# Kernel tuning notes

Measured on AMD Instinct MI355X. Metric: run time of the kernel, lower is better.

The kernel has to match this reference:

```python
import jax, jax.numpy as jnp
import numpy as np

N = 8192
IN_DIM = 256
OUT_DIM = 128
ALPHA = 0.2  # LeakyReLU negative slope
MASK_VAL = -9e15


def setup_inputs() -> dict:
    key = jax.random.key(0)
    k1, k2, k3, k4 = jax.random.split(key, 4)
    adjacency = jax.random.randint(k1, (N, N), 0, 2, dtype=jnp.int32)
    X = jax.random.normal(k2, (N, IN_DIM), dtype=jnp.float32)
    # kaiming-normal-ish scale
    W = jax.random.normal(k3, (IN_DIM, OUT_DIM), dtype=jnp.float32) * np.sqrt(2.0 / IN_DIM)
    a = jax.random.normal(k4, (2 * OUT_DIM, 1), dtype=jnp.float32) * np.sqrt(2.0 / (2 * OUT_DIM))
    return {"adjacency": adjacency, "X": X, "W": W, "a": a}


def reference(adjacency, X, W, a):
    Wh = X @ W  # [N, D]
    # e[i,j] = lrelu([Wh_i ; Wh_j] @ a) = lrelu(Wh@a1 + (Wh@a2)^T)
    a1 = a[:OUT_DIM, 0]   # [D]
    a2 = a[OUT_DIM:, 0]   # [D]
    e = (Wh @ a1)[:, None] + (Wh @ a2)[None, :]  # [N, N]
    e = jax.nn.leaky_relu(e, negative_slope=ALPHA)
    scores = jnp.where(adjacency > 0, e, jnp.asarray(MASK_VAL, e.dtype))
    attention = jax.nn.softmax(scores, axis=1)  # dropout p=0 -> identity
    h_prime = attention @ Wh  # [N, D]
    return jax.nn.elu(h_prime)
```

## Files before the change

### kernel.cpp

```cpp
#include <hip/hip_runtime.h>
#include <hip/hip_bf16.h>

#define NN 8192
#define KDIM 256
#define DDIM 128

typedef __attribute__((ext_vector_type(8))) short short8;
typedef __attribute__((ext_vector_type(4))) float floatx4;
typedef __attribute__((ext_vector_type(4))) int intx4;

__device__ __forceinline__ unsigned short f2bf(float x) {
    unsigned int u = __float_as_uint(x);
    return (unsigned short)((u + 0x8000u) >> 16);
}

__global__ void k_trip(float* out, float v) {
    if (threadIdx.x == 0 && blockIdx.x == 0) out[0] = v;
}

__global__ void kA_swizzleW(const float* __restrict__ W, unsigned short* __restrict__ WB) {
    int gid = blockIdx.x * blockDim.x + threadIdx.x;
    int kt = gid >> 9, nt = (gid >> 6) & 7, lane = gid & 63;
    int quad = lane >> 4, c = lane & 15;
    short8 pack;
#pragma unroll
    for (int t = 0; t < 8; ++t)
        pack[t] = (short)f2bf(W[(kt * 32 + quad * 8 + t) * DDIM + nt * 16 + c]);
    *(short8*)(WB + ((size_t)(kt * 8 + nt) * 64 + lane) * 8) = pack;
}

__global__ __launch_bounds__(256) void kB_wh(
        const float* __restrict__ X,
        const unsigned short* __restrict__ WB,
        const float* __restrict__ a,
        unsigned short* __restrict__ WhB,
        float* __restrict__ f, float* __restrict__ g) {
    __shared__ unsigned short tile[64 * 128];
    int tid = threadIdx.x;
    int wave = tid >> 6, lane = tid & 63;
    int quad = lane >> 4, c = lane & 15;
    int rowbase = blockIdx.x * 64 + wave * 16;

    floatx4 acc[8];
#pragma unroll
    for (int nt = 0; nt < 8; ++nt) acc[nt] = (floatx4)(0.0f);

    const short8* WB8 = (const short8*)WB;
#pragma unroll
    for (int ks = 0; ks < 8; ++ks) {
        const float* xp = X + (size_t)(rowbase + c) * KDIM + ks * 32 + quad * 8;
        floatx4 x0 = *(const floatx4*)xp;
        floatx4 x1 = *(const floatx4*)(xp + 4);
        short8 afrag;
#pragma unroll
        for (int t = 0; t < 4; ++t) { afrag[t] = (short)f2bf(x0[t]); afrag[4 + t] = (short)f2bf(x1[t]); }
#pragma unroll
        for (int nt = 0; nt < 8; ++nt) {
            short8 b = WB8[(ks * 8 + nt) * 64 + lane];
            acc[nt] = __builtin_amdgcn_mfma_f32_16x16x32_bf16(afrag, b, acc[nt], 0, 0, 0);
        }
    }

    float fp[4] = {0.f, 0.f, 0.f, 0.f}, gp[4] = {0.f, 0.f, 0.f, 0.f};
#pragma unroll
    for (int nt = 0; nt < 8; ++nt) {
        float a1 = a[nt * 16 + c];
        float a2 = a[DDIM + nt * 16 + c];
#pragma unroll
        for (int r = 0; r < 4; ++r) {
            fp[r] += acc[nt][r] * a1;
            gp[r] += acc[nt][r] * a2;
        }
    }
#pragma unroll
    for (int m = 1; m < 16; m <<= 1) {
#pragma unroll
        for (int r = 0; r < 4; ++r) {
            fp[r] += __shfl_xor(fp[r], m);
            gp[r] += __shfl_xor(gp[r], m);
        }
    }
    if (c == 0) {
#pragma unroll
        for (int r = 0; r < 4; ++r) {
            f[rowbase + quad * 4 + r] = fp[r];
            g[rowbase + quad * 4 + r] = gp[r];
        }
    }

#pragma unroll
    for (int nt = 0; nt < 8; ++nt)
#pragma unroll
        for (int r = 0; r < 4; ++r)
            tile[(wave * 16 + quad * 4 + r) * 128 + nt * 16 + c] = f2bf(acc[nt][r]);
    __syncthreads();

    int kt2 = wave >> 1;
#pragma unroll
    for (int ntj = 0; ntj < 4; ++ntj) {
        int nt = (wave & 1) * 4 + ntj;
        short8 pack;
#pragma unroll
        for (int t = 0; t < 8; ++t)
            pack[t] = (short)tile[(kt2 * 32 + quad * 8 + t) * 128 + nt * 16 + c];
        *(short8*)(WhB + ((size_t)((blockIdx.x * 2 + kt2) * 8 + nt) * 64 + lane) * 8) = pack;
    }
}

__global__ __launch_bounds__(256, 3) void kC_attn(
        const int* __restrict__ adj,
        const unsigned short* __restrict__ WhB,
        const float* __restrict__ f, const float* __restrict__ g,
        float* __restrict__ out) {
    __shared__ float smem[8192];
    int tid = threadIdx.x;
    int wave = tid >> 6, lane = tid & 63;
    int quad = lane >> 4, c = lane & 15;
    int rowbase = blockIdx.x * 16;

    for (int i = tid; i < NN / 4; i += 256)
        ((floatx4*)smem)[i] = ((const floatx4*)g)[i];
    __syncthreads();

    float f0 = f[rowbase + c];

    floatx4 acc[8];
#pragma unroll
    for (int nt = 0; nt < 8; ++nt) acc[nt] = (floatx4)(0.0f);
    float l0 = 0.0f;

    const intx4* arow = (const intx4*)(adj + (size_t)(rowbase + c) * NN);
    const short8* WhB8 = (const short8*)WhB;

    intx4 A0a = __builtin_nontemporal_load(&arow[(0 * 4 + wave) * 8 + quad * 2]);
    intx4 A0b = __builtin_nontemporal_load(&arow[(0 * 4 + wave) * 8 + quad * 2 + 1]);
    intx4 A1a = __builtin_nontemporal_load(&arow[(1 * 4 + wave) * 8 + quad * 2]);
    intx4 A1b = __builtin_nontemporal_load(&arow[(1 * 4 + wave) * 8 + quad * 2 + 1]);

    short8 bfrA[8], bfrB[8];
#pragma unroll
    for (int nt = 0; nt < 8; ++nt)
        bfrA[nt] = WhB8[((size_t)(0 * 4 + wave) * 8 + nt) * 64 + lane];

#define KC_STEP(ITC, BCUR, BNEXT) do {                                          \
        int j4n_ = (((ITC) + 2) & 63) * 4 + wave;                               \
        intx4 A2a_ = __builtin_nontemporal_load(&arow[j4n_ * 8 + quad * 2]);    \
        intx4 A2b_ = __builtin_nontemporal_load(&arow[j4n_ * 8 + quad * 2 + 1]);\
        int J32n_ = (((ITC) + 1) & 63) * 4 + wave;                              \
        _Pragma("unroll")                                                       \
        for (int nt = 0; nt < 8; ++nt)                                          \
            BNEXT[nt] = WhB8[((size_t)J32n_ * 8 + nt) * 64 + lane];             \
        int J32_ = (ITC) * 4 + wave;                                            \
        int gb_ = J32_ * 32 + quad * 8;                                         \
        floatx4 g0_ = *(const floatx4*)&smem[gb_];                              \
        floatx4 g1_ = *(const floatx4*)&smem[gb_ + 4];                          \
        short8 afr_;                                                            \
        _Pragma("unroll")                                                       \
        for (int u = 0; u < 4; ++u) {                                           \
            float x_, E_;                                                       \
            x_ = f0 + g0_[u]; x_ = fmaxf(x_, 0.2f * x_);                        \
            E_ = (A0a[u] > 0) ? __expf(x_) : 0.0f; l0 += E_;                    \
            afr_[u] = (short)f2bf(E_);                                          \
            x_ = f0 + g1_[u]; x_ = fmaxf(x_, 0.2f * x_);                        \
            E_ = (A0b[u] > 0) ? __expf(x_) : 0.0f; l0 += E_;                    \
            afr_[4 + u] = (short)f2bf(E_);                                      \
        }                                                                       \
        _Pragma("unroll")                                                       \
        for (int nt = 0; nt < 8; ++nt)                                          \
            acc[nt] = __builtin_amdgcn_mfma_f32_16x16x32_bf16(afr_, BCUR[nt],   \
                                                              acc[nt], 0, 0, 0);\
        A0a = A1a; A0b = A1b; A1a = A2a_; A1b = A2b_;                           \
    } while (0)

    for (int it = 0; it < 64; it += 2) {
        KC_STEP(it, bfrA, bfrB);
        KC_STEP(it + 1, bfrB, bfrA);
    }
#undef KC_STEP

    __syncthreads();
    smem[7000 + wave * 64 + lane] = l0;
    __syncthreads();
    if (tid < 16) {
        float s = 0.0f;
#pragma unroll
        for (int w = 0; w < 4; ++w)
#pragma unroll
            for (int q = 0; q < 4; ++q)
                s += smem[7000 + w * 64 + q * 16 + tid];
        smem[7256 + tid] = (s > 0.0f) ? 1.0f / s : 0.0f;
    }
    __syncthreads();

    if (wave >= 2) {
        float* b = &smem[(wave - 2) * 2304 + lane * 36];
#pragma unroll
        for (int nt = 0; nt < 8; ++nt) *(floatx4*)&b[nt * 4] = acc[nt];
    }
    __syncthreads();
    if (wave < 2) {
        float* b = &smem[wave * 2304 + lane * 36];
#pragma unroll
        for (int nt = 0; nt < 8; ++nt) acc[nt] += *(const floatx4*)&b[nt * 4];
    }
    __syncthreads();
    if (wave == 1) {
        float* b = &smem[lane * 36];
#pragma unroll
        for (int nt = 0; nt < 8; ++nt) *(floatx4*)&b[nt * 4] = acc[nt];
    }
    __syncthreads();

    if (wave == 0) {
        float* b = &smem[lane * 36];
#pragma unroll
        for (int nt = 0; nt < 8; ++nt) acc[nt] += *(const floatx4*)&b[nt * 4];
        float linv[4];
#pragma unroll
        for (int r = 0; r < 4; ++r) linv[r] = smem[7256 + quad * 4 + r];
#pragma unroll
        for (int nt = 0; nt < 8; ++nt)
#pragma unroll
            for (int r = 0; r < 4; ++r) {
                float h = acc[nt][r] * linv[r];
                h = (h > 0.0f) ? h : expm1f(h);
                out[(size_t)(rowbase + quad * 4 + r) * DDIM + nt * 16 + c] = h;
            }
    }
}

extern "C" void kernel_launch(void* const* d_in, const int* in_sizes, int n_in,
                              void* d_out, int out_size, void* d_ws, size_t ws_size,
                              hipStream_t stream) {
    float* out = (float*)d_out;

    const void *p_adj = nullptr, *p_X = nullptr, *p_W = nullptr, *p_a = nullptr;
    for (int i = 0; i < n_in; ++i) {
        switch (in_sizes[i]) {
            case NN * NN:     p_adj = d_in[i]; break;
            case NN * KDIM:   p_X   = d_in[i]; break;
            case KDIM * DDIM: p_W   = d_in[i]; break;
            case 2 * DDIM:    p_a   = d_in[i]; break;
            default: break;
        }
    }
    if (!p_adj || !p_X || !p_W || !p_a) {
        k_trip<<<dim3(1), dim3(64), 0, stream>>>(out, 99999.0f);
        return;
    }

    size_t off_WB  = 0;
    size_t off_WhB = off_WB + 65536;
    size_t off_f   = off_WhB + (size_t)NN * DDIM * 2;
    size_t off_g   = off_f + NN * 4;
    size_t needed  = off_g + NN * 4;
    if (ws_size < needed) {
        k_trip<<<dim3(1), dim3(64), 0, stream>>>(out, 12345.0f);
        return;
    }
    char* ws = (char*)d_ws;
    unsigned short* WB  = (unsigned short*)(ws + off_WB);
    unsigned short* WhB = (unsigned short*)(ws + off_WhB);
    float*          f   = (float*)(ws + off_f);
    float*          g   = (float*)(ws + off_g);

    const int*   adj = (const int*)p_adj;
    const float* X   = (const float*)p_X;
    const float* W   = (const float*)p_W;
    const float* a   = (const float*)p_a;

    kA_swizzleW<<<dim3(16), dim3(256), 0, stream>>>(W, WB);
    kB_wh<<<dim3(128), dim3(256), 0, stream>>>(X, WB, a, WhB, f, g);
    kC_attn<<<dim3(512), dim3(256), 0, stream>>>(adj, WhB, f, g, out);
}
```

Measured before the change: 474.5 us.

## Split attention column range across two blocks and merge partials in new kernel

```diff
diff --git a/kernel.cpp b/kernel.cpp
--- a/kernel.cpp
+++ b/kernel.cpp
@@ -107,19 +107,24 @@
     }
 }
 
-__global__ __launch_bounds__(256, 3) void kC_attn(
+__global__ __launch_bounds__(256, 4) void kC_attn(
         const int* __restrict__ adj,
         const unsigned short* __restrict__ WhB,
         const float* __restrict__ f, const float* __restrict__ g,
-        float* __restrict__ out) {
+        float* __restrict__ pacc, float* __restrict__ pl) {
     __shared__ float smem[8192];
     int tid = threadIdx.x;
     int wave = tid >> 6, lane = tid & 63;
     int quad = lane >> 4, c = lane & 15;
-    int rowbase = blockIdx.x * 16;
-
-    for (int i = tid; i < NN / 4; i += 256)
-        ((floatx4*)smem)[i] = ((const floatx4*)g)[i];
+    int bq   = blockIdx.x >> 9;
+    int brow = blockIdx.x & 511;
+    int rowbase = brow * 16;
+
+    {
+        const floatx4* g4 = (const floatx4*)g;
+        for (int i = tid; i < 1024; i += 256)
+            ((floatx4*)smem)[i] = g4[bq * 1024 + i];
+    }
     __syncthreads();
 
     float f0 = f[rowbase + c];
@@ -131,27 +136,27 @@
 
     const intx4* arow = (const intx4*)(adj + (size_t)(rowbase + c) * NN);
     const short8* WhB8 = (const short8*)WhB;
-
-    intx4 A0a = __builtin_nontemporal_load(&arow[(0 * 4 + wave) * 8 + quad * 2]);
-    intx4 A0b = __builtin_nontemporal_load(&arow[(0 * 4 + wave) * 8 + quad * 2 + 1]);
-    intx4 A1a = __builtin_nontemporal_load(&arow[(1 * 4 + wave) * 8 + quad * 2]);
-    intx4 A1b = __builtin_nontemporal_load(&arow[(1 * 4 + wave) * 8 + quad * 2 + 1]);
+    int jbase = bq * 128;
+
+    intx4 A0a = arow[(jbase + 0 * 4 + wave) * 8 + quad * 2];
+    intx4 A0b = arow[(jbase + 0 * 4 + wave) * 8 + quad * 2 + 1];
+    intx4 A1a = arow[(jbase + 1 * 4 + wave) * 8 + quad * 2];
+    intx4 A1b = arow[(jbase + 1 * 4 + wave) * 8 + quad * 2 + 1];
 
     short8 bfrA[8], bfrB[8];
 #pragma unroll
     for (int nt = 0; nt < 8; ++nt)
-        bfrA[nt] = WhB8[((size_t)(0 * 4 + wave) * 8 + nt) * 64 + lane];
+        bfrA[nt] = WhB8[((size_t)(jbase + wave) * 8 + nt) * 64 + lane];
 
 #define KC_STEP(ITC, BCUR, BNEXT) do {                                          \
-        int j4n_ = (((ITC) + 2) & 63) * 4 + wave;                               \
-        intx4 A2a_ = __builtin_nontemporal_load(&arow[j4n_ * 8 + quad * 2]);    \
-        intx4 A2b_ = __builtin_nontemporal_load(&arow[j4n_ * 8 + quad * 2 + 1]);\
-        int J32n_ = (((ITC) + 1) & 63) * 4 + wave;                              \
+        int j4n_ = jbase + (((ITC) + 2) & 31) * 4 + wave;                       \
+        intx4 A2a_ = arow[j4n_ * 8 + quad * 2];                                 \
+        intx4 A2b_ = arow[j4n_ * 8 + quad * 2 + 1];                             \
+        int J32n_ = jbase + (((ITC) + 1) & 31) * 4 + wave;                      \
         _Pragma("unroll")                                                       \
         for (int nt = 0; nt < 8; ++nt)                                          \
             BNEXT[nt] = WhB8[((size_t)J32n_ * 8 + nt) * 64 + lane];             \
-        int J32_ = (ITC) * 4 + wave;                                            \
-        int gb_ = J32_ * 32 + quad * 8;                                         \
+        int gb_ = ((ITC) * 4 + wave) * 32 + quad * 8;                           \
         floatx4 g0_ = *(const floatx4*)&smem[gb_];                              \
         floatx4 g1_ = *(const floatx4*)&smem[gb_ + 4];                          \
         short8 afr_;                                                            \
@@ -172,7 +177,7 @@
         A0a = A1a; A0b = A1b; A1a = A2a_; A1b = A2b_;                           \
     } while (0)
 
-    for (int it = 0; it < 64; it += 2) {
+    for (int it = 0; it < 32; it += 2) {
         KC_STEP(it, bfrA, bfrB);
         KC_STEP(it + 1, bfrB, bfrA);
     }
@@ -188,9 +193,8 @@
 #pragma unroll
             for (int q = 0; q < 4; ++q)
                 s += smem[7000 + w * 64 + q * 16 + tid];
-        smem[7256 + tid] = (s > 0.0f) ? 1.0f / s : 0.0f;
-    }
-    __syncthreads();
+        pl[bq * NN + rowbase + tid] = s;
+    }
 
     if (wave >= 2) {
         float* b = &smem[(wave - 2) * 2304 + lane * 36];
@@ -215,18 +219,32 @@
         float* b = &smem[lane * 36];
 #pragma unroll
         for (int nt = 0; nt < 8; ++nt) acc[nt] += *(const floatx4*)&b[nt * 4];
-        float linv[4];
-#pragma unroll
-        for (int r = 0; r < 4; ++r) linv[r] = smem[7256 + quad * 4 + r];
+        float* pb = pacc + (size_t)bq * NN * DDIM;
 #pragma unroll
         for (int nt = 0; nt < 8; ++nt)
 #pragma unroll
-            for (int r = 0; r < 4; ++r) {
-                float h = acc[nt][r] * linv[r];
-                h = (h > 0.0f) ? h : expm1f(h);
-                out[(size_t)(rowbase + quad * 4 + r) * DDIM + nt * 16 + c] = h;
-            }
-    }
+            for (int r = 0; r < 4; ++r)
+                pb[(size_t)(rowbase + quad * 4 + r) * DDIM + nt * 16 + c] = acc[nt][r];
+    }
+}
+
+__global__ __launch_bounds__(256) void kD_merge(
+        const float* __restrict__ pacc, const float* __restrict__ pl,
+        float* __restrict__ out) {
+    int i = blockIdx.x * 256 + threadIdx.x;
+    const floatx4* p4 = (const floatx4*)pacc;
+    floatx4 a = p4[i];
+    floatx4 b = p4[i + NN * DDIM / 4];
+    int row = i >> 5;
+    float s = pl[row] + pl[NN + row];
+    float inv = (s > 0.0f) ? 1.0f / s : 0.0f;
+    floatx4 h;
+#pragma unroll
+    for (int r = 0; r < 4; ++r) {
+        float v = (a[r] + b[r]) * inv;
+        h[r] = (v > 0.0f) ? v : expm1f(v);
+    }
+    ((floatx4*)out)[i] = h;
 }
 
 extern "C" void kernel_launch(void* const* d_in, const int* in_sizes, int n_in,
@@ -249,20 +267,24 @@
         return;
     }
 
-    size_t off_WB  = 0;
-    size_t off_WhB = off_WB + 65536;
-    size_t off_f   = off_WhB + (size_t)NN * DDIM * 2;
-    size_t off_g   = off_f + NN * 4;
-    size_t needed  = off_g + NN * 4;
+    size_t off_WB   = 0;
+    size_t off_WhB  = off_WB + 65536;
+    size_t off_f    = off_WhB + (size_t)NN * DDIM * 2;
+    size_t off_g    = off_f + NN * 4;
+    size_t off_pacc = off_g + NN * 4;
+    size_t off_pl   = off_pacc + (size_t)2 * NN * DDIM * 4;
+    size_t needed   = off_pl + (size_t)2 * NN * 4;
     if (ws_size < needed) {
         k_trip<<<dim3(1), dim3(64), 0, stream>>>(out, 12345.0f);
         return;
     }
     char* ws = (char*)d_ws;
-    unsigned short* WB  = (unsigned short*)(ws + off_WB);
-    unsigned short* WhB = (unsigned short*)(ws + off_WhB);
-    float*          f   = (float*)(ws + off_f);
-    float*          g   = (float*)(ws + off_g);
+    unsigned short* WB   = (unsigned short*)(ws + off_WB);
+    unsigned short* WhB  = (unsigned short*)(ws + off_WhB);
+    float*          f    = (float*)(ws + off_f);
+    float*          g    = (float*)(ws + off_g);
+    float*          pacc = (float*)(ws + off_pacc);
+    float*          pl   = (float*)(ws + off_pl);
 
     const int*   adj = (const int*)p_adj;
     const float* X   = (const float*)p_X;
@@ -271,5 +293,6 @@
 
     kA_swizzleW<<<dim3(16), dim3(256), 0, stream>>>(W, WB);
     kB_wh<<<dim3(128), dim3(256), 0, stream>>>(X, WB, a, WhB, f, g);
-    kC_attn<<<dim3(512), dim3(256), 0, stream>>>(adj, WhB, f, g, out);
-}
+    kC_attn<<<dim3(1024), dim3(256), 0, stream>>>(adj, WhB, f, g, pacc, pl);
+    kD_merge<<<dim3(NN * DDIM / 4 / 256), dim3(256), 0, stream>>>(pacc, pl, out);
+}
```

Result: faster. 430.9 us (-9.2%).
